# Optimization experiments

Measured on AMD Instinct MI355X. Metric: run time of the kernel, lower is better.

Reference implementation:

```python
import jax, jax.numpy as jnp
import numpy as np

N = 8192      # number of tree nodes
IN = 1024     # in_dim
M = 1024      # effective mem_dim = 2 * mem_dim_init
K = 8         # max children (complete 8-ary tree)


def _linear_init(key, out_dim, in_dim):
    k1, k2 = jax.random.split(key)
    s = 1.0 / np.sqrt(in_dim)
    w = jax.random.uniform(k1, (out_dim, in_dim), minval=-s, maxval=s, dtype=jnp.float32)
    b = jax.random.uniform(k2, (out_dim,), minval=-s, maxval=s, dtype=jnp.float32)
    return w, b


def setup_inputs() -> dict:
    key = jax.random.key(0)
    ks = jax.random.split(key, 5)
    w_ioux, b_ioux = _linear_init(ks[0], 3 * M, IN)
    w_iouh, b_iouh = _linear_init(ks[1], 3 * M, M)
    w_fx, b_fx = _linear_init(ks[2], M, IN)
    w_fh, b_fh = _linear_init(ks[3], M, M)
    inputs = jax.random.normal(ks[4], (N, IN), dtype=jnp.float32)
    # Complete K-ary tree: children of node p are p*K+1 .. p*K+K (clipped).
    # Pad with index N, which addresses an always-zero dummy row.
    ch = np.full((N, K), N, dtype=np.int32)
    for j in range(K):
        idx = np.arange(N) * K + 1 + j
        valid = idx < N
        ch[valid, j] = idx[valid]
    return dict(inputs=inputs, children=jnp.asarray(ch),
                w_ioux=w_ioux, b_ioux=b_ioux, w_iouh=w_iouh, b_iouh=b_iouh,
                w_fx=w_fx, b_fx=b_fx, w_fh=w_fh, b_fh=b_fh)


def reference(inputs, children, w_ioux, b_ioux, w_iouh, b_iouh, w_fx, b_fx, w_fh, b_fh):
    # Precompute the input-side projections for all nodes at once.
    iou_x = inputs @ w_ioux.T + b_ioux   # [N, 3M]
    fx_x = inputs @ w_fx.T + b_fx        # [N, M]
    h0 = jnp.zeros((N + 1, M), inputs.dtype)  # row N is the zero pad slot
    c0 = jnp.zeros((N + 1, M), inputs.dtype)

    def step(carry, t):
        h_buf, c_buf = carry
        ch = children[t]           # [K] child indices (pad = N -> zero rows)
        ch_h = h_buf[ch]           # [K, M] real child h's
        ch_c = c_buf[ch]           # [K, M] real child c's
        # Faithful to original: for internal nodes child_c/child_h are SWAPPED,
        # so the 'child_h_sum' and f-gate inputs use the real c's, while the
        # forgotten memory (fc) multiplies the real h's. Leaves: all zeros.
        csum = ch_c.sum(0)                                   # [M]
        iou = iou_x[t] + csum @ w_iouh.T + b_iouh            # [3M]
        i_g, o_g, u_g = jnp.split(iou, 3)
        i_g = jax.nn.sigmoid(i_g)
        o_g = jax.nn.sigmoid(o_g)
        u_g = jnp.tanh(u_g)
        f = jax.nn.sigmoid(ch_c @ w_fh.T + b_fh + fx_x[t])   # [K, M]
        c = i_g * u_g + (f * ch_h).sum(0)                    # [M]
        h = o_g * jnp.tanh(c)
        return (h_buf.at[t].set(h), c_buf.at[t].set(c)), None

    # Children always have larger indices than their parent, so processing
    # t = N-1 .. 0 matches the original reverse-BFS (leaves-first) order.
    order = jnp.arange(N - 1, -1, -1)
    (h_buf, c_buf), _ = jax.lax.scan(step, (h0, c0), order)
    root_h = h_buf[0][None, :]   # [1, M]
    root_c = c_buf[0][None, :]   # [1, M]
    return root_h, root_c
```

## Files before the change

### kernel.cpp

```cpp
#include <hip/hip_runtime.h>

typedef __bf16 bf16x8 __attribute__((ext_vector_type(8)));
typedef __attribute__((ext_vector_type(4))) float f4;

#define AS1 __attribute__((address_space(1)))
#define AS3 __attribute__((address_space(3)))

__device__ __forceinline__ unsigned short f2bf(float f) {
    union { float f; unsigned int u; } x; x.f = f;
    return (unsigned short)((x.u + 0x7fffu + ((x.u >> 16) & 1u)) >> 16);
}
__device__ __forceinline__ float bf2f(unsigned short u) {
    union { unsigned int u; float f; } x; x.u = (unsigned int)u << 16;
    return x.f;
}
__device__ __forceinline__ float fsigm(float x) {
    return __builtin_amdgcn_rcpf(1.f + __expf(-x));
}
__device__ __forceinline__ float ftanh(float x) {
    return 1.f - 2.f * __builtin_amdgcn_rcpf(1.f + __expf(2.f * x));
}
__device__ __forceinline__ void gload_lds16(const unsigned short* g, unsigned short* l) {
    __builtin_amdgcn_global_load_lds((const AS1 unsigned int*)g, (AS3 unsigned int*)l, 16, 0, 0);
}
__device__ __forceinline__ void bar() {
    asm volatile("" ::: "memory");
    __builtin_amdgcn_s_barrier();
    asm volatile("" ::: "memory");
}

__global__ void prep_all_k(const float* __restrict__ inputs, const float* __restrict__ w_ioux,
                           const float* __restrict__ w_fx, const float* __restrict__ w_iouh,
                           const float* __restrict__ w_fh,
                           const float* __restrict__ b_ioux, const float* __restrict__ b_iouh,
                           const float* __restrict__ b_fx, const float* __restrict__ b_fh,
                           unsigned short* __restrict__ Xbf, unsigned short* __restrict__ Wiouxbf,
                           unsigned short* __restrict__ Wfxbf, unsigned short* __restrict__ Whbf,
                           unsigned short* __restrict__ Wfhbf,
                           float* __restrict__ bias_iou, float* __restrict__ bias_f,
                           unsigned short* __restrict__ c_bf, unsigned short* __restrict__ h_bf) {
    int b = blockIdx.x;
    if (b < 16384) {
        int idx = b * 256 + threadIdx.x;
        const float* src; unsigned short* dst; int rel;
        if (idx < 2097152)      { src = inputs; dst = Xbf;     rel = idx; }
        else if (idx < 2883584) { src = w_ioux; dst = Wiouxbf; rel = idx - 2097152; }
        else if (idx < 3145728) { src = w_fx;   dst = Wfxbf;   rel = idx - 2883584; }
        else if (idx < 3932160) { src = w_iouh; dst = Whbf;    rel = idx - 3145728; }
        else                    { src = w_fh;   dst = Wfhbf;   rel = idx - 3932160; }
        float4 v = reinterpret_cast<const float4*>(src)[rel];
        ushort4 o; o.x = f2bf(v.x); o.y = f2bf(v.y); o.z = f2bf(v.z); o.w = f2bf(v.w);
        reinterpret_cast<ushort4*>(dst)[rel] = o;
    } else if (b < 16400) {
        int idx = (b - 16384) * 256 + threadIdx.x;
        if (idx < 3072) bias_iou[idx] = b_ioux[idx] + b_iouh[idx];
        else { int j = idx - 3072; bias_f[j] = b_fx[j] + b_fh[j]; }
    } else {
        int j = (b - 16400) * 256 + threadIdx.x;
        size_t o = (size_t)8192 * 1024 + j;
        c_bf[o] = 0; h_bf[o] = 0;
    }
}

__device__ __forceinline__ void stage_half(const unsigned short* __restrict__ G, int trow0, int kt,
                                           unsigned short* lds_region, int tid) {
#pragma unroll
    for (int ii = 0; ii < 2; ++ii) {
        int c = ii * 512 + tid;
        int r = c >> 3, sl = c & 7;
        gload_lds16(G + (size_t)(trow0 + r) * 1024 + kt * 64 + ((sl ^ (r & 7)) * 8),
                    lds_region + c * 8);
    }
}
__device__ __forceinline__ bf16x8 rdfrag(const unsigned short* region, int rowih, int kslot) {
    return *reinterpret_cast<const bf16x8*>(&region[rowih * 64 + ((kslot ^ (rowih & 7)) * 8)]);
}

#define RD_A(AF, REG, FB)                                                        \
    _Pragma("unroll") for (int f_ = 0; f_ < 4; ++f_)                             \
    _Pragma("unroll") for (int s_ = 0; s_ < 2; ++s_)                             \
        (AF)[f_][s_] = rdfrag((REG), ((FB) + f_) * 16 + fr, s_ * 4 + q);
#define RD_B(BQ, REG, GB)                                                        \
    _Pragma("unroll") for (int g_ = 0; g_ < 2; ++g_)                             \
    _Pragma("unroll") for (int s_ = 0; s_ < 2; ++s_)                             \
        (BQ)[g_][s_] = rdfrag((REG), bcol0 + ((GB) + g_) * 16 + fr, s_ * 4 + q);
#define MF16(FB, GB, AF, BQ)                                                     \
    __builtin_amdgcn_s_setprio(1);                                               \
    _Pragma("unroll") for (int s_ = 0; s_ < 2; ++s_)                             \
    _Pragma("unroll") for (int f_ = 0; f_ < 4; ++f_)                             \
    _Pragma("unroll") for (int g_ = 0; g_ < 2; ++g_)                             \
        acc[(FB) + f_][(GB) + g_] = __builtin_amdgcn_mfma_f32_16x16x32_bf16(     \
            (AF)[f_][s_], (BQ)[g_][s_], acc[(FB) + f_][(GB) + g_], 0, 0, 0);     \
    __builtin_amdgcn_s_setprio(0);

__global__ __launch_bounds__(512, 2)
void gemm_big_k(const unsigned short* __restrict__ Xbf, const unsigned short* __restrict__ Wioux,
                const unsigned short* __restrict__ Wfx,
                const float* __restrict__ bias_iou, const float* __restrict__ bias_f,
                unsigned short* __restrict__ P_iou, unsigned short* __restrict__ P_f) {
    __shared__ unsigned short ls[65536];
    int b = blockIdx.x;
    b = (b & 7) * 50 + (b >> 3);
    const unsigned short* Am; const unsigned short* Bm; unsigned short* Cp; const float* biasp;
    int tm, tn, ldc;
    if (b < 384) {
        tm = (b & 31) * 256; tn = (b >> 5) * 256;
        Am = Xbf; Bm = Wioux; Cp = P_iou; biasp = bias_iou; ldc = 3072;
    } else {
        int bb = b - 384;
        tm = (bb & 3) * 256; tn = (bb >> 2) * 256;
        Am = Xbf; Bm = Wfx; Cp = P_f; biasp = bias_f; ldc = 1024;
    }
    const int tid = threadIdx.x;
    const int l = tid & 63, w = tid >> 6;
    const int wm = w >> 2, wn = w & 3;
    const int fr = l & 15, q = l >> 4;
    const int bcol0 = (wn & 1) * 64;

    unsigned short* S0 = ls;
    unsigned short* S1 = ls + 32768;
    const unsigned short* Ar0 = S0 + wm * 8192;
    const unsigned short* Br0 = S0 + (2 + (wn >> 1)) * 8192;
    const unsigned short* Ar1 = S1 + wm * 8192;
    const unsigned short* Br1 = S1 + (2 + (wn >> 1)) * 8192;

    f4 acc[8][4];
#pragma unroll
    for (int i = 0; i < 8; ++i)
#pragma unroll
        for (int j = 0; j < 4; ++j) acc[i][j] = (f4){0.f, 0.f, 0.f, 0.f};

    stage_half(Am, tm,       0, S0 + 0 * 8192, tid);
    stage_half(Am, tm + 128, 0, S0 + 1 * 8192, tid);
    stage_half(Bm, tn,       0, S0 + 2 * 8192, tid);
    stage_half(Bm, tn + 128, 0, S0 + 3 * 8192, tid);
    stage_half(Bm, tn,       1, S1 + 2 * 8192, tid);
    stage_half(Bm, tn + 128, 1, S1 + 3 * 8192, tid);
    asm volatile("s_waitcnt vmcnt(4)" ::: "memory");
    bar();

    for (int i = 0; i < 8; ++i) {
        bf16x8 afA[4][2], afB[4][2], bq01[2][2], bq23[2][2];
        RD_A(afA, Ar0, 0)
        RD_B(bq01, Br0, 0)
        stage_half(Am, tm,       2 * i + 1, S1 + 0 * 8192, tid);
        bar();
        MF16(0, 0, afA, bq01)
        bar();
        RD_B(bq23, Br0, 2)
        stage_half(Am, tm + 128, 2 * i + 1, S1 + 1 * 8192, tid);
        bar();
        MF16(0, 2, afA, bq23)
        bar();
        RD_A(afB, Ar0, 4)
        if (i < 7) stage_half(Bm, tn,       2 * i + 2, S0 + 2 * 8192, tid);
        bar();
        MF16(4, 2, afB, bq23)
        bar();
        if (i < 7) {
            stage_half(Bm, tn + 128, 2 * i + 2, S0 + 3 * 8192, tid);
            asm volatile("s_waitcnt vmcnt(4)" ::: "memory");
        } else {
            asm volatile("s_waitcnt vmcnt(0)" ::: "memory");
        }
        bar();
        MF16(4, 0, afB, bq01)
        bar();
        RD_A(afA, Ar1, 0)
        RD_B(bq01, Br1, 0)
        if (i < 7) stage_half(Am, tm,       2 * i + 2, S0 + 0 * 8192, tid);
        bar();
        MF16(0, 0, afA, bq01)
        bar();
        RD_B(bq23, Br1, 2)
        if (i < 7) stage_half(Am, tm + 128, 2 * i + 2, S0 + 1 * 8192, tid);
        bar();
        MF16(0, 2, afA, bq23)
        bar();
        RD_A(afB, Ar1, 4)
        if (i < 7) stage_half(Bm, tn,       2 * i + 3, S1 + 2 * 8192, tid);
        bar();
        MF16(4, 2, afB, bq23)
        bar();
        if (i < 7) {
            stage_half(Bm, tn + 128, 2 * i + 3, S1 + 3 * 8192, tid);
            asm volatile("s_waitcnt vmcnt(4)" ::: "memory");
        } else {
            asm volatile("s_waitcnt vmcnt(0)" ::: "memory");
        }
        bar();
        MF16(4, 0, afB, bq01)
        bar();
    }

#pragma unroll
    for (int f = 0; f < 8; ++f)
#pragma unroll
        for (int g = 0; g < 4; ++g) {
            int col = tn + wn * 64 + g * 16 + fr;
            float bv = biasp[col];
#pragma unroll
            for (int r = 0; r < 4; ++r) {
                int row = tm + wm * 128 + f * 16 + q * 4 + r;
                Cp[(size_t)row * ldc + col] = f2bf(acc[f][g][r] + bv);
            }
        }
}

__device__ __forceinline__ void gemm_core_db(const unsigned short* __restrict__ A,
                                             const unsigned short* __restrict__ B,
                                             int M, int tile_m, int tile_n, int kb, int nsteps,
                                             unsigned short* lsA, unsigned short* lsB,
                                             f4 acc[4][4]) {
    const int K = 1024;
    const int tid = threadIdx.x;
    const int l = tid & 63, wid = tid >> 6;
    const int wm = wid >> 1, wn = wid & 1;
    const int fr = l & 15, q = l >> 4;

#pragma unroll
    for (int i = 0; i < 4; ++i)
#pragma unroll
        for (int j = 0; j < 4; ++j) acc[i][j] = (f4){0.f, 0.f, 0.f, 0.f};

    const unsigned short* ga[4]; const unsigned short* gb[4];
    unsigned short *la[4], *lb[4];
#pragma unroll
    for (int i = 0; i < 4; ++i) {
        int chunk = i * 256 + tid;
        int row = chunk >> 3, slot = chunk & 7;
        int scol = (slot ^ (row & 7)) * 8;
        ga[i] = A + (size_t)min(tile_m + row, M - 1) * K + kb * 64 + scol;
        gb[i] = B + (size_t)(tile_n + row) * K + kb * 64 + scol;
        la[i] = lsA + chunk * 8;
        lb[i] = lsB + chunk * 8;
    }
#pragma unroll
    for (int i = 0; i < 4; ++i) gload_lds16(ga[i], la[i]);
#pragma unroll
    for (int i = 0; i < 4; ++i) gload_lds16(gb[i], lb[i]);

    int roffA[4], roffB[4];
#pragma unroll
    for (int f = 0; f < 4; ++f) {
        roffA[f] = (wm * 64 + f * 16 + fr) * 64;
        roffB[f] = (wn * 64 + f * 16 + fr) * 64;
    }
    const int sw = fr & 7;
    int cur = 0;
    for (int t = 0; t < nsteps; ++t) {
        if (t < nsteps - 1) {
            int k0 = (t + 1) * 64;
            int nb = (cur ^ 1) * 8192;
#pragma unroll
            for (int i = 0; i < 4; ++i) gload_lds16(ga[i] + k0, la[i] + nb);
#pragma unroll
            for (int i = 0; i < 4; ++i) gload_lds16(gb[i] + k0, lb[i] + nb);
            asm volatile("s_waitcnt vmcnt(8)" ::: "memory");
        } else {
            asm volatile("s_waitcnt vmcnt(0)" ::: "memory");
        }
        __builtin_amdgcn_s_barrier();
        const unsigned short* bA = lsA + cur * 8192;
        const unsigned short* bB = lsB + cur * 8192;
        bf16x8 af[4][2], bq[4][2];
#pragma unroll
        for (int f = 0; f < 4; ++f)
#pragma unroll
            for (int s = 0; s < 2; ++s) {
                int sl = ((s * 4 + q) ^ sw) * 8;
                af[f][s] = *reinterpret_cast<const bf16x8*>(&bA[roffA[f] + sl]);
                bq[f][s] = *reinterpret_cast<const bf16x8*>(&bB[roffB[f] + sl]);
            }
#pragma unroll
        for (int s = 0; s < 2; ++s)
#pragma unroll
            for (int i = 0; i < 4; ++i)
#pragma unroll
                for (int j = 0; j < 4; ++j)
                    acc[i][j] = __builtin_amdgcn_mfma_f32_16x16x32_bf16(af[i][s], bq[j][s], acc[i][j], 0, 0, 0);
        __builtin_amdgcn_s_barrier();
        cur ^= 1;
    }
}

__global__ void leaf_act_k(const unsigned short* __restrict__ P_iou,
                           unsigned short* __restrict__ h_bf, unsigned short* __restrict__ c_bf) {
    int idx = blockIdx.x * blockDim.x + threadIdx.x;
    int t = 1024 + (idx >> 8);
    int j = (idx & 255) * 4;
    const unsigned short* p = P_iou + (size_t)t * 3072 + j;
    ushort4 pi = *reinterpret_cast<const ushort4*>(p);
    ushort4 po = *reinterpret_cast<const ushort4*>(p + 1024);
    ushort4 pu = *reinterpret_cast<const ushort4*>(p + 2048);
    ushort4 cb, hb;
    float c0, c1, c2, c3;
    c0 = fsigm(bf2f(pi.x)) * ftanh(bf2f(pu.x)); hb.x = f2bf(fsigm(bf2f(po.x)) * ftanh(c0)); cb.x = f2bf(c0);
    c1 = fsigm(bf2f(pi.y)) * ftanh(bf2f(pu.y)); hb.y = f2bf(fsigm(bf2f(po.y)) * ftanh(c1)); cb.y = f2bf(c1);
    c2 = fsigm(bf2f(pi.z)) * ftanh(bf2f(pu.z)); hb.z = f2bf(fsigm(bf2f(po.z)) * ftanh(c2)); cb.z = f2bf(c2);
    c3 = fsigm(bf2f(pi.w)) * ftanh(bf2f(pu.w)); hb.w = f2bf(fsigm(bf2f(po.w)) * ftanh(c3)); cb.w = f2bf(c3);
    size_t o = (size_t)t * 1024 + j;
    *reinterpret_cast<ushort4*>(c_bf + o) = cb;
    *reinterpret_cast<ushort4*>(h_bf + o) = hb;
}

__device__ __forceinline__ void csum_dev(const unsigned short* __restrict__ c_bf,
                                         unsigned short* __restrict__ csum_bf, int lo, int w) {
    int tt = w >> 8, j = (w & 255) * 4;
    int t = lo + tt;
    size_t base = (size_t)(t * 8 + 1) * 1024 + j;
    float s0 = 0.f, s1 = 0.f, s2 = 0.f, s3 = 0.f;
#pragma unroll
    for (int k = 0; k < 8; ++k) {
        ushort4 v = *reinterpret_cast<const ushort4*>(c_bf + base + (size_t)k * 1024);
        s0 += bf2f(v.x); s1 += bf2f(v.y); s2 += bf2f(v.z); s3 += bf2f(v.w);
    }
    ushort4 o; o.x = f2bf(s0); o.y = f2bf(s1); o.z = f2bf(s2); o.w = f2bf(s3);
    *reinterpret_cast<ushort4*>(csum_bf + (size_t)t * 1024 + j) = o;
}

__global__ void csum_k(const unsigned short* __restrict__ c_bf, unsigned short* __restrict__ csum_bf,
                       int lo, int n) {
    int w = blockIdx.x * blockDim.x + threadIdx.x;
    if (w < n * 256) csum_dev(c_bf, csum_bf, lo, w);
}

__global__ void node_update_k(const unsigned short* __restrict__ P_iou,
                              const unsigned short* __restrict__ P_f,
                              const float* __restrict__ out_iouh, const float* __restrict__ out_f,
                              unsigned short* __restrict__ h_bf, unsigned short* __restrict__ c_bf,
                              float* __restrict__ out, int lo, int n) {
    int w = blockIdx.x * blockDim.x + threadIdx.x;
    if (w >= n * 256) return;
    int tt = w >> 8, j = (w & 255) * 4;
    int t = lo + tt;
    const unsigned short* p = P_iou + (size_t)t * 3072 + j;
    ushort4 pi4 = *reinterpret_cast<const ushort4*>(p);
    ushort4 po4 = *reinterpret_cast<const ushort4*>(p + 1024);
    ushort4 pu4 = *reinterpret_cast<const ushort4*>(p + 2048);
    const float* oi = out_iouh + (size_t)tt * 3072 + j;
    f4 oii = *reinterpret_cast<const f4*>(oi);
    f4 oio = *reinterpret_cast<const f4*>(oi + 1024);
    f4 oiu = *reinterpret_cast<const f4*>(oi + 2048);
    ushort4 pf4 = *reinterpret_cast<const ushort4*>(P_f + (size_t)t * 1024 + j);
    float pf[4] = {bf2f(pf4.x), bf2f(pf4.y), bf2f(pf4.z), bf2f(pf4.w)};
    float a[4], og[4];
    a[0] = fsigm(bf2f(pi4.x) + oii[0]) * ftanh(bf2f(pu4.x) + oiu[0]);
    a[1] = fsigm(bf2f(pi4.y) + oii[1]) * ftanh(bf2f(pu4.y) + oiu[1]);
    a[2] = fsigm(bf2f(pi4.z) + oii[2]) * ftanh(bf2f(pu4.z) + oiu[2]);
    a[3] = fsigm(bf2f(pi4.w) + oii[3]) * ftanh(bf2f(pu4.w) + oiu[3]);
    og[0] = fsigm(bf2f(po4.x) + oio[0]);
    og[1] = fsigm(bf2f(po4.y) + oio[1]);
    og[2] = fsigm(bf2f(po4.z) + oio[2]);
    og[3] = fsigm(bf2f(po4.w) + oio[3]);
#pragma unroll
    for (int k = 0; k < 8; ++k) {
        f4 fo = *reinterpret_cast<const f4*>(out_f + (size_t)(tt * 8 + k) * 1024 + j);
        ushort4 hc = *reinterpret_cast<const ushort4*>(h_bf + (size_t)(t * 8 + 1 + k) * 1024 + j);
        a[0] += fsigm(pf[0] + fo[0]) * bf2f(hc.x);
        a[1] += fsigm(pf[1] + fo[1]) * bf2f(hc.y);
        a[2] += fsigm(pf[2] + fo[2]) * bf2f(hc.z);
        a[3] += fsigm(pf[3] + fo[3]) * bf2f(hc.w);
    }
    float h0 = og[0] * ftanh(a[0]);
    float h1 = og[1] * ftanh(a[1]);
    float h2 = og[2] * ftanh(a[2]);
    float h3 = og[3] * ftanh(a[3]);
    size_t o = (size_t)t * 1024 + j;
    ushort4 cb; cb.x = f2bf(a[0]); cb.y = f2bf(a[1]); cb.z = f2bf(a[2]); cb.w = f2bf(a[3]);
    ushort4 hb; hb.x = f2bf(h0); hb.y = f2bf(h1); hb.z = f2bf(h2); hb.w = f2bf(h3);
    *reinterpret_cast<ushort4*>(c_bf + o) = cb;
    *reinterpret_cast<ushort4*>(h_bf + o) = hb;
    if (t == 0) {
        f4 hv = {h0, h1, h2, h3};
        f4 cv = {a[0], a[1], a[2], a[3]};
        *reinterpret_cast<f4*>(out + j) = hv;
        *reinterpret_cast<f4*>(out + 1024 + j) = cv;
    }
}

struct GDesc {
    const unsigned short* A;
    const unsigned short* B;
    float* C;
    int M;
    int ldc;
    int tiles_n;
    int tiles_total;
};

__global__ __launch_bounds__(256)
void gemm_dual_k(GDesc d0, GDesc d1) {
    __shared__ unsigned short lsA[16384];
    __shared__ unsigned short lsB[16384];
    int b = blockIdx.x;
    GDesc d; int bb;
    if (b < d0.tiles_total) { d = d0; bb = b; }
    else { d = d1; bb = b - d0.tiles_total; }
    const int tile_m = (bb / d.tiles_n) * 128;
    const int tile_n = (bb % d.tiles_n) * 128;
    f4 acc[4][4];
    gemm_core_db(d.A, d.B, d.M, tile_m, tile_n, 0, 16, lsA, lsB, acc);

    const int l = threadIdx.x & 63, wid = threadIdx.x >> 6;
    const int wm = wid >> 1, wn = wid & 1;
    const int fr = l & 15, q = l >> 4;
#pragma unroll
    for (int i = 0; i < 4; ++i)
#pragma unroll
        for (int j = 0; j < 4; ++j) {
            int col = tile_n + wn * 64 + fr + j * 16;
#pragma unroll
            for (int r = 0; r < 4; ++r) {
                int row = tile_m + wm * 64 + q * 4 + i * 16 + r;
                if (row < d.M) d.C[(size_t)row * d.ldc + col] = acc[i][j][r];
            }
        }
}

__global__ __launch_bounds__(256)
void gemm_tail_k(const unsigned short* __restrict__ csum_lvl,
                 const unsigned short* __restrict__ cchild,
                 const unsigned short* __restrict__ Whbf, const unsigned short* __restrict__ Wfhbf,
                 float* __restrict__ part_iouh, float* __restrict__ part_f, int n) {
    __shared__ unsigned short lsA[16384];
    __shared__ unsigned short lsB[16384];
    int b = blockIdx.x;
    const unsigned short* A; const unsigned short* Bw; float* C;
    int M, ldc, tm, tn, split;
    if (b < 96) {
        split = b & 3; int tile = b >> 2;
        A = csum_lvl; Bw = Whbf; M = n; ldc = 3072; tm = 0; tn = tile * 128;
        C = part_iouh + (size_t)split * 64 * 3072;
    } else {
        int bb = b - 96;
        split = bb & 3; int tile = bb >> 2;
        A = cchild; Bw = Wfhbf; M = 8 * n; ldc = 1024;
        tm = (tile >> 3) * 128; tn = (tile & 7) * 128;
        C = part_f + (size_t)split * 512 * 1024;
    }
    f4 acc[4][4];
    gemm_core_db(A, Bw, M, tm, tn, split * 4, 4, lsA, lsB, acc);

    const int l = threadIdx.x & 63, wid = threadIdx.x >> 6;
    const int wm = wid >> 1, wn = wid & 1;
    const int fr = l & 15, q = l >> 4;
#pragma unroll
    for (int i = 0; i < 4; ++i)
#pragma unroll
        for (int j = 0; j < 4; ++j) {
            int col = tn + wn * 64 + fr + j * 16;
#pragma unroll
            for (int r = 0; r < 4; ++r) {
                int row = tm + wm * 64 + q * 4 + i * 16 + r;
                if (row < M) C[(size_t)row * ldc + col] = acc[i][j][r];
            }
        }
}

__global__ void node_update_tail_k(const unsigned short* __restrict__ P_iou,
                                   const unsigned short* __restrict__ P_f,
                                   const float* __restrict__ part_iouh,
                                   const float* __restrict__ part_f,
                                   unsigned short* __restrict__ h_bf, unsigned short* __restrict__ c_bf,
                                   float* __restrict__ out, int lo, int n) {
    int w = blockIdx.x * blockDim.x + threadIdx.x;
    if (w >= n * 256) return;
    int tt = w >> 8, j = (w & 255) * 4;
    int t = lo + tt;
    f4 oii = {0.f, 0.f, 0.f, 0.f}, oio = oii, oiu = oii;
#pragma unroll
    for (int s = 0; s < 4; ++s) {
        const float* base = part_iouh + (size_t)s * 64 * 3072 + (size_t)tt * 3072 + j;
        oii += *reinterpret_cast<const f4*>(base);
        oio += *reinterpret_cast<const f4*>(base + 1024);
        oiu += *reinterpret_cast<const f4*>(base + 2048);
    }
    const unsigned short* p = P_iou + (size_t)t * 3072 + j;
    ushort4 pi4 = *reinterpret_cast<const ushort4*>(p);
    ushort4 po4 = *reinterpret_cast<const ushort4*>(p + 1024);
    ushort4 pu4 = *reinterpret_cast<const ushort4*>(p + 2048);
    ushort4 pf4 = *reinterpret_cast<const ushort4*>(P_f + (size_t)t * 1024 + j);
    float pf[4] = {bf2f(pf4.x), bf2f(pf4.y), bf2f(pf4.z), bf2f(pf4.w)};
    float a[4], og[4];
    a[0] = fsigm(bf2f(pi4.x) + oii[0]) * ftanh(bf2f(pu4.x) + oiu[0]);
    a[1] = fsigm(bf2f(pi4.y) + oii[1]) * ftanh(bf2f(pu4.y) + oiu[1]);
    a[2] = fsigm(bf2f(pi4.z) + oii[2]) * ftanh(bf2f(pu4.z) + oiu[2]);
    a[3] = fsigm(bf2f(pi4.w) + oii[3]) * ftanh(bf2f(pu4.w) + oiu[3]);
    og[0] = fsigm(bf2f(po4.x) + oio[0]);
    og[1] = fsigm(bf2f(po4.y) + oio[1]);
    og[2] = fsigm(bf2f(po4.z) + oio[2]);
    og[3] = fsigm(bf2f(po4.w) + oio[3]);
#pragma unroll
    for (int k = 0; k < 8; ++k) {
        f4 fo = {0.f, 0.f, 0.f, 0.f};
#pragma unroll
        for (int s = 0; s < 4; ++s)
            fo += *reinterpret_cast<const f4*>(part_f + (size_t)s * 512 * 1024 +
                                               (size_t)(tt * 8 + k) * 1024 + j);
        ushort4 hc = *reinterpret_cast<const ushort4*>(h_bf + (size_t)(t * 8 + 1 + k) * 1024 + j);
        a[0] += fsigm(pf[0] + fo[0]) * bf2f(hc.x);
        a[1] += fsigm(pf[1] + fo[1]) * bf2f(hc.y);
        a[2] += fsigm(pf[2] + fo[2]) * bf2f(hc.z);
        a[3] += fsigm(pf[3] + fo[3]) * bf2f(hc.w);
    }
    float h0 = og[0] * ftanh(a[0]);
    float h1 = og[1] * ftanh(a[1]);
    float h2 = og[2] * ftanh(a[2]);
    float h3 = og[3] * ftanh(a[3]);
    size_t o = (size_t)t * 1024 + j;
    ushort4 cb; cb.x = f2bf(a[0]); cb.y = f2bf(a[1]); cb.z = f2bf(a[2]); cb.w = f2bf(a[3]);
    ushort4 hb; hb.x = f2bf(h0); hb.y = f2bf(h1); hb.z = f2bf(h2); hb.w = f2bf(h3);
    *reinterpret_cast<ushort4*>(c_bf + o) = cb;
    *reinterpret_cast<ushort4*>(h_bf + o) = hb;
    if (t == 0) {
        f4 hv = {h0, h1, h2, h3};
        f4 cv = {a[0], a[1], a[2], a[3]};
        *reinterpret_cast<f4*>(out + j) = hv;
        *reinterpret_cast<f4*>(out + 1024 + j) = cv;
    }
}

extern "C" void kernel_launch(void* const* d_in, const int* in_sizes, int n_in,
                              void* d_out, int out_size, void* d_ws, size_t ws_size,
                              hipStream_t stream) {
    const float* inputs = (const float*)d_in[0];
    const float* w_ioux = (const float*)d_in[2];
    const float* b_ioux = (const float*)d_in[3];
    const float* w_iouh = (const float*)d_in[4];
    const float* b_iouh = (const float*)d_in[5];
    const float* w_fx   = (const float*)d_in[6];
    const float* b_fx   = (const float*)d_in[7];
    const float* w_fh   = (const float*)d_in[8];
    const float* b_fh   = (const float*)d_in[9];
    float* out = (float*)d_out;

    char* ws = (char*)d_ws;
    size_t off = 0;
    auto alloc = [&](size_t bytes) -> void* {
        void* p = ws + off;
        off += (bytes + 255) & ~(size_t)255;
        return p;
    };
    unsigned short* Xbf     = (unsigned short*)alloc((size_t)8192 * 1024 * 2);
    unsigned short* Wiouxbf = (unsigned short*)alloc((size_t)3072 * 1024 * 2);
    unsigned short* Wfxbf   = (unsigned short*)alloc((size_t)1024 * 1024 * 2);
    unsigned short* Whbf    = (unsigned short*)alloc((size_t)3072 * 1024 * 2);
    unsigned short* Wfhbf   = (unsigned short*)alloc((size_t)1024 * 1024 * 2);
    float* bias_iou         = (float*)alloc((size_t)3072 * 4);
    float* bias_f           = (float*)alloc((size_t)1024 * 4);
    unsigned short* P_iou   = (unsigned short*)alloc((size_t)8192 * 3072 * 2);
    unsigned short* P_f     = (unsigned short*)alloc((size_t)1024 * 1024 * 2);
    unsigned short* c_bf    = (unsigned short*)alloc((size_t)8193 * 1024 * 2);
    unsigned short* h_bf    = (unsigned short*)alloc((size_t)8193 * 1024 * 2);
    unsigned short* csum_bf = (unsigned short*)alloc((size_t)1024 * 1024 * 2);
    float* out_iouh         = (float*)alloc((size_t)512 * 3072 * 4);
    float* out_f            = (float*)alloc((size_t)4096 * 1024 * 4);
    float* part_iouh        = (float*)alloc((size_t)4 * 64 * 3072 * 4);
    float* part_f           = (float*)alloc((size_t)4 * 512 * 1024 * 4);

    prep_all_k<<<dim3(16404), dim3(256), 0, stream>>>(
        inputs, w_ioux, w_fx, w_iouh, w_fh, b_ioux, b_iouh, b_fx, b_fh,
        Xbf, Wiouxbf, Wfxbf, Whbf, Wfhbf, bias_iou, bias_f, c_bf, h_bf);

    gemm_big_k<<<dim3(400), dim3(512), 0, stream>>>(Xbf, Wiouxbf, Wfxbf,
                                                    bias_iou, bias_f, P_iou, P_f);
    leaf_act_k<<<dim3(7168), dim3(256), 0, stream>>>(P_iou, h_bf, c_bf);
    csum_k<<<dim3(896), dim3(256), 0, stream>>>(c_bf, csum_bf, 128, 896);

    {
        const int lo = 585, n = 439;
        GDesc d0, d1;
        d0.A = csum_bf + (size_t)lo * 1024; d0.B = Whbf; d0.C = out_iouh;
        d0.M = n; d0.ldc = 3072; d0.tiles_n = 24;
        d0.tiles_total = ((n + 127) / 128) * 24;
        d1.A = c_bf + (size_t)(lo * 8 + 1) * 1024; d1.B = Wfhbf; d1.C = out_f;
        d1.M = 8 * n; d1.ldc = 1024; d1.tiles_n = 8;
        d1.tiles_total = ((8 * n + 127) / 128) * 8;
        gemm_dual_k<<<dim3(d0.tiles_total + d1.tiles_total), dim3(256), 0, stream>>>(d0, d1);
        node_update_k<<<dim3(n), dim3(256), 0, stream>>>(
            P_iou, P_f, out_iouh, out_f, h_bf, c_bf, out, lo, n);
    }
    {
        const int lo = 73, n = 512;
        csum_k<<<dim3(55), dim3(256), 0, stream>>>(c_bf, csum_bf, 73, 55);
        GDesc d0, d1;
        d0.A = csum_bf + (size_t)lo * 1024; d0.B = Whbf; d0.C = out_iouh;
        d0.M = n; d0.ldc = 3072; d0.tiles_n = 24;
        d0.tiles_total = ((n + 127) / 128) * 24;
        d1.A = c_bf + (size_t)(lo * 8 + 1) * 1024; d1.B = Wfhbf; d1.C = out_f;
        d1.M = 8 * n; d1.ldc = 1024; d1.tiles_n = 8;
        d1.tiles_total = ((8 * n + 127) / 128) * 8;
        gemm_dual_k<<<dim3(d0.tiles_total + d1.tiles_total), dim3(256), 0, stream>>>(d0, d1);
        node_update_k<<<dim3(n), dim3(256), 0, stream>>>(
            P_iou, P_f, out_iouh, out_f, h_bf, c_bf, out, lo, n);
    }
    const int T_LO[3] = {9, 1, 0};
    const int T_N[3]  = {64, 8, 1};
    for (int lv = 0; lv < 3; ++lv) {
        int lo = T_LO[lv], n = T_N[lv];
        csum_k<<<dim3(n), dim3(256), 0, stream>>>(c_bf, csum_bf, lo, n);
        int fm_tiles = (8 * n + 127) / 128;
        int nblk = 96 + fm_tiles * 8 * 4;
        gemm_tail_k<<<dim3(nblk), dim3(256), 0, stream>>>(
            csum_bf + (size_t)lo * 1024, c_bf + (size_t)(lo * 8 + 1) * 1024,
            Whbf, Wfhbf, part_iouh, part_f, n);
        node_update_tail_k<<<dim3(n), dim3(256), 0, stream>>>(
            P_iou, P_f, part_iouh, part_f, h_bf, c_bf, out, lo, n);
    }
    (void)in_sizes; (void)n_in; (void)out_size; (void)ws_size;
}
```

Measured before the change: 206.6 us.

## Use 256x256 pipelined GEMM core for level GEMMs and swizzle big-GEMM tiles

Factors the 256x256 8-wave LDS-pipelined GEMM body into a shared core, adds row clamping for partial M tiles, and replaces the 128x128 dual GEMM used for the two large tree levels with a 512-thread 256x256 version. It also remaps big-GEMM block indices into grouped super-tiles so blocks running together share A and B tiles in cache. Bigger tiles cut redundant operand traffic, but the level GEMMs now launch far fewer blocks (about 80-88), which may leave many CUs idle.

```diff
diff --git a/kernel.cpp b/kernel.cpp
--- a/kernel.cpp
+++ b/kernel.cpp
@@ -62,13 +62,14 @@
     }
 }
 
-__device__ __forceinline__ void stage_half(const unsigned short* __restrict__ G, int trow0, int kt,
-                                           unsigned short* lds_region, int tid) {
+__device__ __forceinline__ void stage_half(const unsigned short* __restrict__ G, int M,
+                                           int trow0, int kt, unsigned short* lds_region, int tid) {
 #pragma unroll
     for (int ii = 0; ii < 2; ++ii) {
         int c = ii * 512 + tid;
         int r = c >> 3, sl = c & 7;
-        gload_lds16(G + (size_t)(trow0 + r) * 1024 + kt * 64 + ((sl ^ (r & 7)) * 8),
+        int row = min(trow0 + r, M - 1);
+        gload_lds16(G + (size_t)row * 1024 + kt * 64 + ((sl ^ (r & 7)) * 8),
                     lds_region + c * 8);
     }
 }
@@ -93,6 +94,93 @@
             (AF)[f_][s_], (BQ)[g_][s_], acc[(FB) + f_][(GB) + g_], 0, 0, 0);     \
     __builtin_amdgcn_s_setprio(0);
 
+__device__ __forceinline__ void gemm256_core(const unsigned short* __restrict__ Am,
+                                             const unsigned short* __restrict__ Bm,
+                                             int M, int tm, int tn,
+                                             unsigned short* ls, f4 acc[8][4]) {
+    const int tid = threadIdx.x;
+    const int l = tid & 63, w = tid >> 6;
+    const int wm = w >> 2, wn = w & 3;
+    const int fr = l & 15, q = l >> 4;
+    const int bcol0 = (wn & 1) * 64;
+    const int BIGM = 1 << 30;
+
+    unsigned short* S0 = ls;
+    unsigned short* S1 = ls + 32768;
+    const unsigned short* Ar0 = S0 + wm * 8192;
+    const unsigned short* Br0 = S0 + (2 + (wn >> 1)) * 8192;
+    const unsigned short* Ar1 = S1 + wm * 8192;
+    const unsigned short* Br1 = S1 + (2 + (wn >> 1)) * 8192;
+
+#pragma unroll
+    for (int i = 0; i < 8; ++i)
+#pragma unroll
+        for (int j = 0; j < 4; ++j) acc[i][j] = (f4){0.f, 0.f, 0.f, 0.f};
+
+    stage_half(Am, M, tm,       0, S0 + 0 * 8192, tid);
+    stage_half(Am, M, tm + 128, 0, S0 + 1 * 8192, tid);
+    stage_half(Bm, BIGM, tn,       0, S0 + 2 * 8192, tid);
+    stage_half(Bm, BIGM, tn + 128, 0, S0 + 3 * 8192, tid);
+    stage_half(Bm, BIGM, tn,       1, S1 + 2 * 8192, tid);
+    stage_half(Bm, BIGM, tn + 128, 1, S1 + 3 * 8192, tid);
+    asm volatile("s_waitcnt vmcnt(4)" ::: "memory");
+    bar();
+
+    for (int i = 0; i < 8; ++i) {
+        bf16x8 afA[4][2], afB[4][2], bq01[2][2], bq23[2][2];
+        RD_A(afA, Ar0, 0)
+        RD_B(bq01, Br0, 0)
+        stage_half(Am, M, tm,       2 * i + 1, S1 + 0 * 8192, tid);
+        bar();
+        MF16(0, 0, afA, bq01)
+        bar();
+        RD_B(bq23, Br0, 2)
+        stage_half(Am, M, tm + 128, 2 * i + 1, S1 + 1 * 8192, tid);
+        bar();
+        MF16(0, 2, afA, bq23)
+        bar();
+        RD_A(afB, Ar0, 4)
+        if (i < 7) stage_half(Bm, BIGM, tn,       2 * i + 2, S0 + 2 * 8192, tid);
+        bar();
+        MF16(4, 2, afB, bq23)
+        bar();
+        if (i < 7) {
+            stage_half(Bm, BIGM, tn + 128, 2 * i + 2, S0 + 3 * 8192, tid);
+            asm volatile("s_waitcnt vmcnt(4)" ::: "memory");
+        } else {
+            asm volatile("s_waitcnt vmcnt(0)" ::: "memory");
+        }
+        bar();
+        MF16(4, 0, afB, bq01)
+        bar();
+        RD_A(afA, Ar1, 0)
+        RD_B(bq01, Br1, 0)
+        if (i < 7) stage_half(Am, M, tm,       2 * i + 2, S0 + 0 * 8192, tid);
+        bar();
+        MF16(0, 0, afA, bq01)
+        bar();
+        RD_B(bq23, Br1, 2)
+        if (i < 7) stage_half(Am, M, tm + 128, 2 * i + 2, S0 + 1 * 8192, tid);
+        bar();
+        MF16(0, 2, afA, bq23)
+        bar();
+        RD_A(afB, Ar1, 4)
+        if (i < 7) stage_half(Bm, BIGM, tn,       2 * i + 3, S1 + 2 * 8192, tid);
+        bar();
+        MF16(4, 2, afB, bq23)
+        bar();
+        if (i < 7) {
+            stage_half(Bm, BIGM, tn + 128, 2 * i + 3, S1 + 3 * 8192, tid);
+            asm volatile("s_waitcnt vmcnt(4)" ::: "memory");
+        } else {
+            asm volatile("s_waitcnt vmcnt(0)" ::: "memory");
+        }
+        bar();
+        MF16(4, 0, afB, bq01)
+        bar();
+    }
+}
+
 __global__ __launch_bounds__(512, 2)
 void gemm_big_k(const unsigned short* __restrict__ Xbf, const unsigned short* __restrict__ Wioux,
                 const unsigned short* __restrict__ Wfx,
@@ -101,98 +189,24 @@
     __shared__ unsigned short ls[65536];
     int b = blockIdx.x;
     b = (b & 7) * 50 + (b >> 3);
-    const unsigned short* Am; const unsigned short* Bm; unsigned short* Cp; const float* biasp;
+    const unsigned short* Bm; unsigned short* Cp; const float* biasp;
     int tm, tn, ldc;
     if (b < 384) {
-        tm = (b & 31) * 256; tn = (b >> 5) * 256;
-        Am = Xbf; Bm = Wioux; Cp = P_iou; biasp = bias_iou; ldc = 3072;
+        int st = b / 24, wt = b % 24;
+        tm = ((st >> 2) * 8 + wt / 3) * 256;
+        tn = ((st & 3) * 3 + wt % 3) * 256;
+        Bm = Wioux; Cp = P_iou; biasp = bias_iou; ldc = 3072;
     } else {
         int bb = b - 384;
         tm = (bb & 3) * 256; tn = (bb >> 2) * 256;
-        Am = Xbf; Bm = Wfx; Cp = P_f; biasp = bias_f; ldc = 1024;
-    }
-    const int tid = threadIdx.x;
-    const int l = tid & 63, w = tid >> 6;
+        Bm = Wfx; Cp = P_f; biasp = bias_f; ldc = 1024;
+    }
+    f4 acc[8][4];
+    gemm256_core(Xbf, Bm, 8192, tm, tn, ls, acc);
+
+    const int l = threadIdx.x & 63, w = threadIdx.x >> 6;
     const int wm = w >> 2, wn = w & 3;
     const int fr = l & 15, q = l >> 4;
-    const int bcol0 = (wn & 1) * 64;
-
-    unsigned short* S0 = ls;
-    unsigned short* S1 = ls + 32768;
-    const unsigned short* Ar0 = S0 + wm * 8192;
-    const unsigned short* Br0 = S0 + (2 + (wn >> 1)) * 8192;
-    const unsigned short* Ar1 = S1 + wm * 8192;
-    const unsigned short* Br1 = S1 + (2 + (wn >> 1)) * 8192;
-
-    f4 acc[8][4];
-#pragma unroll
-    for (int i = 0; i < 8; ++i)
-#pragma unroll
-        for (int j = 0; j < 4; ++j) acc[i][j] = (f4){0.f, 0.f, 0.f, 0.f};
-
-    stage_half(Am, tm,       0, S0 + 0 * 8192, tid);
-    stage_half(Am, tm + 128, 0, S0 + 1 * 8192, tid);
-    stage_half(Bm, tn,       0, S0 + 2 * 8192, tid);
-    stage_half(Bm, tn + 128, 0, S0 + 3 * 8192, tid);
-    stage_half(Bm, tn,       1, S1 + 2 * 8192, tid);
-    stage_half(Bm, tn + 128, 1, S1 + 3 * 8192, tid);
-    asm volatile("s_waitcnt vmcnt(4)" ::: "memory");
-    bar();
-
-    for (int i = 0; i < 8; ++i) {
-        bf16x8 afA[4][2], afB[4][2], bq01[2][2], bq23[2][2];
-        RD_A(afA, Ar0, 0)
-        RD_B(bq01, Br0, 0)
-        stage_half(Am, tm,       2 * i + 1, S1 + 0 * 8192, tid);
-        bar();
-        MF16(0, 0, afA, bq01)
-        bar();
-        RD_B(bq23, Br0, 2)
-        stage_half(Am, tm + 128, 2 * i + 1, S1 + 1 * 8192, tid);
-        bar();
-        MF16(0, 2, afA, bq23)
-        bar();
-        RD_A(afB, Ar0, 4)
-        if (i < 7) stage_half(Bm, tn,       2 * i + 2, S0 + 2 * 8192, tid);
-        bar();
-        MF16(4, 2, afB, bq23)
-        bar();
-        if (i < 7) {
-            stage_half(Bm, tn + 128, 2 * i + 2, S0 + 3 * 8192, tid);
-            asm volatile("s_waitcnt vmcnt(4)" ::: "memory");
-        } else {
-            asm volatile("s_waitcnt vmcnt(0)" ::: "memory");
-        }
-        bar();
-        MF16(4, 0, afB, bq01)
-        bar();
-        RD_A(afA, Ar1, 0)
-        RD_B(bq01, Br1, 0)
-        if (i < 7) stage_half(Am, tm,       2 * i + 2, S0 + 0 * 8192, tid);
-        bar();
-        MF16(0, 0, afA, bq01)
-        bar();
-        RD_B(bq23, Br1, 2)
-        if (i < 7) stage_half(Am, tm + 128, 2 * i + 2, S0 + 1 * 8192, tid);
-        bar();
-        MF16(0, 2, afA, bq23)
-        bar();
-        RD_A(afB, Ar1, 4)
-        if (i < 7) stage_half(Bm, tn,       2 * i + 3, S1 + 2 * 8192, tid);
-        bar();
-        MF16(4, 2, afB, bq23)
-        bar();
-        if (i < 7) {
-            stage_half(Bm, tn + 128, 2 * i + 3, S1 + 3 * 8192, tid);
-            asm volatile("s_waitcnt vmcnt(4)" ::: "memory");
-        } else {
-            asm volatile("s_waitcnt vmcnt(0)" ::: "memory");
-        }
-        bar();
-        MF16(4, 0, afB, bq01)
-        bar();
-    }
-
 #pragma unroll
     for (int f = 0; f < 8; ++f)
 #pragma unroll
@@ -203,6 +217,44 @@
             for (int r = 0; r < 4; ++r) {
                 int row = tm + wm * 128 + f * 16 + q * 4 + r;
                 Cp[(size_t)row * ldc + col] = f2bf(acc[f][g][r] + bv);
+            }
+        }
+}
+
+struct LDesc {
+    const unsigned short* A;
+    const unsigned short* B;
+    float* C;
+    int M;
+    int tiles_n;
+    int ldc;
+    int tiles_total;
+};
+
+__global__ __launch_bounds__(512, 2)
+void gemm_lvl_k(LDesc d0, LDesc d1) {
+    __shared__ unsigned short ls[65536];
+    int b = blockIdx.x;
+    LDesc d; int bb;
+    if (b < d0.tiles_total) { d = d0; bb = b; }
+    else { d = d1; bb = b - d0.tiles_total; }
+    const int tm = (bb / d.tiles_n) * 256;
+    const int tn = (bb % d.tiles_n) * 256;
+    f4 acc[8][4];
+    gemm256_core(d.A, d.B, d.M, tm, tn, ls, acc);
+
+    const int l = threadIdx.x & 63, w = threadIdx.x >> 6;
+    const int wm = w >> 2, wn = w & 3;
+    const int fr = l & 15, q = l >> 4;
+#pragma unroll
+    for (int f = 0; f < 8; ++f)
+#pragma unroll
+        for (int g = 0; g < 4; ++g) {
+            int col = tn + wn * 64 + g * 16 + fr;
+#pragma unroll
+            for (int r = 0; r < 4; ++r) {
+                int row = tm + wm * 128 + f * 16 + q * 4 + r;
+                if (row < d.M) d.C[(size_t)row * d.ldc + col] = acc[f][g][r];
             }
         }
 }
@@ -379,45 +431,6 @@
     }
 }
 
-struct GDesc {
-    const unsigned short* A;
-    const unsigned short* B;
-    float* C;
-    int M;
-    int ldc;
-    int tiles_n;
-    int tiles_total;
-};
-
-__global__ __launch_bounds__(256)
-void gemm_dual_k(GDesc d0, GDesc d1) {
-    __shared__ unsigned short lsA[16384];
-    __shared__ unsigned short lsB[16384];
-    int b = blockIdx.x;
-    GDesc d; int bb;
-    if (b < d0.tiles_total) { d = d0; bb = b; }
-    else { d = d1; bb = b - d0.tiles_total; }
-    const int tile_m = (bb / d.tiles_n) * 128;
-    const int tile_n = (bb % d.tiles_n) * 128;
-    f4 acc[4][4];
-    gemm_core_db(d.A, d.B, d.M, tile_m, tile_n, 0, 16, lsA, lsB, acc);
-
-    const int l = threadIdx.x & 63, wid = threadIdx.x >> 6;
-    const int wm = wid >> 1, wn = wid & 1;
-    const int fr = l & 15, q = l >> 4;
-#pragma unroll
-    for (int i = 0; i < 4; ++i)
-#pragma unroll
-        for (int j = 0; j < 4; ++j) {
-            int col = tile_n + wn * 64 + fr + j * 16;
-#pragma unroll
-            for (int r = 0; r < 4; ++r) {
-                int row = tile_m + wm * 64 + q * 4 + i * 16 + r;
-                if (row < d.M) d.C[(size_t)row * d.ldc + col] = acc[i][j][r];
-            }
-        }
-}
-
 __global__ __launch_bounds__(256)
 void gemm_tail_k(const unsigned short* __restrict__ csum_lvl,
                  const unsigned short* __restrict__ cchild,
@@ -570,28 +583,24 @@
 
     {
         const int lo = 585, n = 439;
-        GDesc d0, d1;
+        LDesc d0, d1;
         d0.A = csum_bf + (size_t)lo * 1024; d0.B = Whbf; d0.C = out_iouh;
-        d0.M = n; d0.ldc = 3072; d0.tiles_n = 24;
-        d0.tiles_total = ((n + 127) / 128) * 24;
+        d0.M = n; d0.tiles_n = 12; d0.ldc = 3072; d0.tiles_total = 2 * 12;
         d1.A = c_bf + (size_t)(lo * 8 + 1) * 1024; d1.B = Wfhbf; d1.C = out_f;
-        d1.M = 8 * n; d1.ldc = 1024; d1.tiles_n = 8;
-        d1.tiles_total = ((8 * n + 127) / 128) * 8;
-        gemm_dual_k<<<dim3(d0.tiles_total + d1.tiles_total), dim3(256), 0, stream>>>(d0, d1);
+        d1.M = 8 * n; d1.tiles_n = 4; d1.ldc = 1024; d1.tiles_total = 14 * 4;
+        gemm_lvl_k<<<dim3(d0.tiles_total + d1.tiles_total), dim3(512), 0, stream>>>(d0, d1);
         node_update_k<<<dim3(n), dim3(256), 0, stream>>>(
             P_iou, P_f, out_iouh, out_f, h_bf, c_bf, out, lo, n);
     }
     {
         const int lo = 73, n = 512;
         csum_k<<<dim3(55), dim3(256), 0, stream>>>(c_bf, csum_bf, 73, 55);
-        GDesc d0, d1;
+        LDesc d0, d1;
         d0.A = csum_bf + (size_t)lo * 1024; d0.B = Whbf; d0.C = out_iouh;
-        d0.M = n; d0.ldc = 3072; d0.tiles_n = 24;
-        d0.tiles_total = ((n + 127) / 128) * 24;
+        d0.M = n; d0.tiles_n = 12; d0.ldc = 3072; d0.tiles_total = 2 * 12;
         d1.A = c_bf + (size_t)(lo * 8 + 1) * 1024; d1.B = Wfhbf; d1.C = out_f;
-        d1.M = 8 * n; d1.ldc = 1024; d1.tiles_n = 8;
-        d1.tiles_total = ((8 * n + 127) / 128) * 8;
-        gemm_dual_k<<<dim3(d0.tiles_total + d1.tiles_total), dim3(256), 0, stream>>>(d0, d1);
+        d1.M = 8 * n; d1.tiles_n = 4; d1.ldc = 1024; d1.tiles_total = 16 * 4;
+        gemm_lvl_k<<<dim3(d0.tiles_total + d1.tiles_total), dim3(512), 0, stream>>>(d0, d1);
         node_update_k<<<dim3(n), dim3(256), 0, stream>>>(
             P_iou, P_f, out_iouh, out_f, h_bf, c_bf, out, lo, n);
     }
```

Measured after the change: 214.5 us. 3.9% more time.
